# Performance work log

Measured on AMD Instinct MI355X. Metric: run time of the kernel, lower is better.

## Reference

```python
import jax, jax.numpy as jnp
import numpy as np

N_NODES = 10000
N_EDGES = 160000
NF = 512  # node_features
DIMS = [1, 2 * NF // 8, 4 * NF // 8, NF]  # 1 -> 128 -> 256 -> 512


def setup_inputs() -> dict:
    key = jax.random.key(0)
    ks = jax.random.split(key, 10)
    inp = {
        "x": jax.random.normal(ks[0], (N_NODES, 1), dtype=jnp.float32),
        "edge_index": jax.random.randint(ks[1], (2, N_EDGES), 0, N_NODES, dtype=jnp.int64),
        "edge_weights": jax.random.uniform(ks[2], (N_EDGES,), dtype=jnp.float32),
    }
    # Glorot-style init for GCNConv linear weights, zero biases (PyG default)
    for i in range(3):
        d_in, d_out = DIMS[i], DIMS[i + 1]
        scale = (6.0 / (d_in + d_out)) ** 0.5
        inp[f"W{i+1}"] = jax.random.uniform(ks[3 + i], (d_in, d_out), dtype=jnp.float32, minval=-scale, maxval=scale)
        inp[f"b{i+1}"] = jnp.zeros((d_out,), dtype=jnp.float32)
    return inp


def _gcn_layer(h, W, b, src, dst, ew):
    # GCNConv with add_self_loops=False, normalize=False:
    #   h' = scatter_sum(edge_weight * (h @ W)[src] -> dst) + b
    h = h @ W                                    # [N, d_out]
    msg = h[src] * ew[:, None]                   # [E, d_out] gather + scale
    agg = jax.ops.segment_sum(msg, dst, num_segments=N_NODES)  # scatter-add
    return agg + b


def reference(x, edge_index, edge_weights, W1, b1, W2, b2, W3, b3):
    src, dst = edge_index[0], edge_index[1]  # source_to_target flow
    h = _gcn_layer(x, W1, b1, src, dst, edge_weights)
    h = _gcn_layer(h, W2, b2, src, dst, edge_weights)
    h = _gcn_layer(h, W3, b3, src, dst, edge_weights)
    return jax.nn.sigmoid(h)
```

## Files before the change

### kernel.cpp

```cpp
#include <hip/hip_runtime.h>
#include <math.h>

#define N_NODES 10000
#define N_EDGES 160000
#define NCHUNK 32
#define EPC (N_EDGES / NCHUNK)
#define GPC (EPC / 4)


__global__ __launch_bounds__(512) void edges_l1_kernel(
        const int* __restrict__ src, const int* __restrict__ dst,
        const float* __restrict__ ew, const float* __restrict__ x,
        float* __restrict__ s1_part, float* __restrict__ deg_part,
        const float* __restrict__ W1, const float* __restrict__ b1,
        const float* __restrict__ W2,
        float* __restrict__ u_part, float* __restrict__ v_part) {
    int tid = threadIdx.x;
    int blk = blockIdx.x;
    if (blk < 64) {
        __shared__ float lds[N_NODES];
        for (int g = tid; g < N_NODES / 4; g += 512)
            ((float4*)lds)[g] = make_float4(0.f, 0.f, 0.f, 0.f);
        __syncthreads();
        int b = blk & 31;
        bool is_s1 = (blk < 32);
        int base = b * GPC;
        for (int g = tid; g < GPC; g += 512) {
            int4   d4 = ((const int4*)dst)[base + g];
            float4 w4 = ((const float4*)ew)[base + g];
            if (is_s1) {
                int4 s4 = ((const int4*)src)[base + g];
                atomicAdd(&lds[d4.x], w4.x * x[s4.x]);
                atomicAdd(&lds[d4.y], w4.y * x[s4.y]);
                atomicAdd(&lds[d4.z], w4.z * x[s4.z]);
                atomicAdd(&lds[d4.w], w4.w * x[s4.w]);
            } else {
                atomicAdd(&lds[d4.x], w4.x);
                atomicAdd(&lds[d4.y], w4.y);
                atomicAdd(&lds[d4.z], w4.z);
                atomicAdd(&lds[d4.w], w4.w);
            }
        }
        __syncthreads();
        float* dstp = (is_s1 ? s1_part : deg_part) + b * N_NODES;
        for (int g = tid; g < N_NODES / 4; g += 512)
            ((float4*)dstp)[g] = ((float4*)lds)[g];
    } else {
        int b = blk - 64;
        if (tid < 256) {
            int j0 = b * 8;
            float uu = 0.f, vv = 0.f;
            #pragma unroll
            for (int jj = 0; jj < 8; ++jj) {
                float w2 = W2[(j0 + jj) * 256 + tid];
                uu = fmaf(W1[j0 + jj], w2, uu);
                vv = fmaf(b1[j0 + jj], w2, vv);
            }
            u_part[b * 256 + tid] = uu;
            v_part[b * 256 + tid] = vv;
        }
    }
}

__global__ __launch_bounds__(512) void reduce_l1_kernel(
        const float* __restrict__ s1_part, const float* __restrict__ deg_part,
        float* __restrict__ s1, float* __restrict__ deg,
        const float* __restrict__ u_part, const float* __restrict__ v_part,
        const float* __restrict__ b2, const float* __restrict__ W3,
        float* __restrict__ p_part, float* __restrict__ q_part,
        float* __restrict__ r_part) {
    int tid = threadIdx.x;
    int blk = blockIdx.x;
    if (blk < 10) {
        int gid = blk * 512 + tid;
        if (gid < N_NODES / 4) {
            float4 a = make_float4(0.f, 0.f, 0.f, 0.f);
            #pragma unroll
            for (int b = 0; b < NCHUNK; ++b) {
                float4 v = ((const float4*)(s1_part + b * N_NODES))[gid];
                a.x += v.x; a.y += v.y; a.z += v.z; a.w += v.w;
            }
            ((float4*)s1)[gid] = a;
        } else if (gid < 2 * (N_NODES / 4)) {
            int c = gid - N_NODES / 4;
            float4 a = make_float4(0.f, 0.f, 0.f, 0.f);
            #pragma unroll
            for (int b = 0; b < NCHUNK; ++b) {
                float4 v = ((const float4*)(deg_part + b * N_NODES))[c];
                a.x += v.x; a.y += v.y; a.z += v.z; a.w += v.w;
            }
            ((float4*)deg)[c] = a;
        }
    } else {
        int c = blk - 10;
        __shared__ float su[16], sv[16], sb[16];
        if (tid < 16) {
            int kk = c * 16 + tid;
            float uu = 0.f, vv = 0.f;
            #pragma unroll
            for (int b = 0; b < 16; ++b) {
                uu += u_part[b * 256 + kk];
                vv += v_part[b * 256 + kk];
            }
            su[tid] = uu; sv[tid] = vv; sb[tid] = b2[kk];
        }
        __syncthreads();
        float pp = 0.f, qq = 0.f, rr = 0.f;
        #pragma unroll
        for (int kk = 0; kk < 16; ++kk) {
            float w3 = W3[(c * 16 + kk) * 512 + tid];
            pp = fmaf(su[kk], w3, pp);
            qq = fmaf(sv[kk], w3, qq);
            rr = fmaf(sb[kk], w3, rr);
        }
        p_part[c * 512 + tid] = pp;
        q_part[c * 512 + tid] = qq;
        r_part[c * 512 + tid] = rr;
    }
}

__global__ __launch_bounds__(512) void edges_l2_kernel(
        const int* __restrict__ src, const int* __restrict__ dst,
        const float* __restrict__ ew,
        const float* __restrict__ s1, const float* __restrict__ deg,
        float* __restrict__ t2_part, float* __restrict__ B_part) {
    int tid = threadIdx.x;
    int blk = blockIdx.x;
    __shared__ float lds[N_NODES];
    for (int g = tid; g < N_NODES / 4; g += 512)
        ((float4*)lds)[g] = make_float4(0.f, 0.f, 0.f, 0.f);
    __syncthreads();
    int b = blk & 31;
    const float* gsrc = (blk < 32) ? s1 : deg;
    int base = b * GPC;
    for (int g = tid; g < GPC; g += 512) {
        int4   s4 = ((const int4*)src)[base + g];
        int4   d4 = ((const int4*)dst)[base + g];
        float4 w4 = ((const float4*)ew)[base + g];
        atomicAdd(&lds[d4.x], w4.x * gsrc[s4.x]);
        atomicAdd(&lds[d4.y], w4.y * gsrc[s4.y]);
        atomicAdd(&lds[d4.z], w4.z * gsrc[s4.z]);
        atomicAdd(&lds[d4.w], w4.w * gsrc[s4.w]);
    }
    __syncthreads();
    float* dstp = ((blk < 32) ? t2_part : B_part) + b * N_NODES;
    for (int g = tid; g < N_NODES / 4; g += 512)
        ((float4*)dstp)[g] = ((float4*)lds)[g];
}

__global__ __launch_bounds__(512) void reduce_l2_kernel(
        const float* __restrict__ t2_part, const float* __restrict__ B_part,
        float* __restrict__ t2, float* __restrict__ Bf,
        const float* __restrict__ p_part, const float* __restrict__ q_part,
        const float* __restrict__ r_part,
        float* __restrict__ p, float* __restrict__ q, float* __restrict__ r) {
    int tid = threadIdx.x;
    int blk = blockIdx.x;
    if (blk < 10) {
        int gid = blk * 512 + tid;
        if (gid < N_NODES / 4) {
            float4 a = make_float4(0.f, 0.f, 0.f, 0.f);
            #pragma unroll
            for (int b = 0; b < NCHUNK; ++b) {
                float4 v = ((const float4*)(t2_part + b * N_NODES))[gid];
                a.x += v.x; a.y += v.y; a.z += v.z; a.w += v.w;
            }
            ((float4*)t2)[gid] = a;
        } else if (gid < 2 * (N_NODES / 4)) {
            int c = gid - N_NODES / 4;
            float4 a = make_float4(0.f, 0.f, 0.f, 0.f);
            #pragma unroll
            for (int b = 0; b < NCHUNK; ++b) {
                float4 v = ((const float4*)(B_part + b * N_NODES))[c];
                a.x += v.x; a.y += v.y; a.z += v.z; a.w += v.w;
            }
            ((float4*)Bf)[c] = a;
        }
    } else {
        float pp = 0.f, qq = 0.f, rr = 0.f;
        #pragma unroll
        for (int c = 0; c < 16; ++c) {
            pp += p_part[c * 512 + tid];
            qq += q_part[c * 512 + tid];
            rr += r_part[c * 512 + tid];
        }
        p[tid] = pp; q[tid] = qq; r[tid] = rr;
    }
}

__global__ __launch_bounds__(512) void edges_l3_kernel(
        const int* __restrict__ src, const int* __restrict__ dst,
        const float* __restrict__ ew, const float* __restrict__ t2,
        float* __restrict__ A_part) {
    int tid = threadIdx.x;
    int b = blockIdx.x;
    __shared__ float lds[N_NODES];
    for (int g = tid; g < N_NODES / 4; g += 512)
        ((float4*)lds)[g] = make_float4(0.f, 0.f, 0.f, 0.f);
    __syncthreads();
    int base = b * GPC;
    for (int g = tid; g < GPC; g += 512) {
        int4   s4 = ((const int4*)src)[base + g];
        int4   d4 = ((const int4*)dst)[base + g];
        float4 w4 = ((const float4*)ew)[base + g];
        atomicAdd(&lds[d4.x], w4.x * t2[s4.x]);
        atomicAdd(&lds[d4.y], w4.y * t2[s4.y]);
        atomicAdd(&lds[d4.z], w4.z * t2[s4.z]);
        atomicAdd(&lds[d4.w], w4.w * t2[s4.w]);
    }
    __syncthreads();
    float* dstp = A_part + b * N_NODES;
    for (int g = tid; g < N_NODES / 4; g += 512)
        ((float4*)dstp)[g] = ((float4*)lds)[g];
}

__global__ __launch_bounds__(256) void output_kernel(
        const float* __restrict__ A_part, const float* __restrict__ Bf,
        const float* __restrict__ deg,
        const float* __restrict__ p, const float* __restrict__ q,
        const float* __restrict__ r, const float* __restrict__ b3,
        float* __restrict__ out) {
    int tid = threadIdx.x;
    int n0 = blockIdx.x * 16;
    __shared__ float sA[256];
    __shared__ float A_l[16], B_l[16], D_l[16];
    {
        int c = tid & 15, rr = tid >> 4;
        sA[tid] = A_part[rr * N_NODES + n0 + c] +
                  A_part[(rr + 16) * N_NODES + n0 + c];
    }
    __syncthreads();
    if (tid < 16) {
        float s = 0.f;
        #pragma unroll
        for (int b = 0; b < 16; ++b) s += sA[b * 16 + tid];
        A_l[tid] = s;
        B_l[tid] = Bf[n0 + tid];
        D_l[tid] = deg[n0 + tid];
    }
    __syncthreads();
    #pragma unroll
    for (int h = 0; h < 8; ++h) {
        int idx = h * 256 + tid;
        int nl = idx >> 7;
        int j = idx & 127;
        float a = A_l[nl], b = B_l[nl], dg = D_l[nl];
        float4 P = ((const float4*)p)[j];
        float4 Q = ((const float4*)q)[j];
        float4 R = ((const float4*)r)[j];
        float4 B3 = ((const float4*)b3)[j];
        float4 o;
        float zx = fmaf(a, P.x, fmaf(b, Q.x, fmaf(dg, R.x, B3.x)));
        float zy = fmaf(a, P.y, fmaf(b, Q.y, fmaf(dg, R.y, B3.y)));
        float zz = fmaf(a, P.z, fmaf(b, Q.z, fmaf(dg, R.z, B3.z)));
        float zw = fmaf(a, P.w, fmaf(b, Q.w, fmaf(dg, R.w, B3.w)));
        o.x = 1.f / (1.f + __expf(-zx));
        o.y = 1.f / (1.f + __expf(-zy));
        o.z = 1.f / (1.f + __expf(-zz));
        o.w = 1.f / (1.f + __expf(-zw));
        ((float4*)out)[(size_t)(n0 + nl) * 128 + j] = o;
    }
}

extern "C" void kernel_launch(void* const* d_in, const int* in_sizes, int n_in,
                              void* d_out, int out_size, void* d_ws, size_t ws_size,
                              hipStream_t stream) {
    const float* x  = (const float*)d_in[0];
    const int*   ei = (const int*)d_in[1];
    const float* ew = (const float*)d_in[2];
    const float* W1 = (const float*)d_in[3];
    const float* b1 = (const float*)d_in[4];
    const float* W2 = (const float*)d_in[5];
    const float* b2 = (const float*)d_in[6];
    const float* W3 = (const float*)d_in[7];
    const float* b3 = (const float*)d_in[8];
    float* out = (float*)d_out;

    float* ws       = (float*)d_ws;
    float* s1       = ws;
    float* deg      = ws + 10000;
    float* t2       = ws + 20000;
    float* Bf       = ws + 30000;
    float* p        = ws + 40000;
    float* q        = ws + 40512;
    float* r        = ws + 41024;
    float* u_part   = ws + 42000;
    float* v_part   = ws + 46096;
    float* p_part   = ws + 50192;
    float* q_part   = ws + 58384;
    float* r_part   = ws + 66576;
    float* s1_part  = ws + 80000;
    float* deg_part = ws + 400000;
    float* t2_part  = ws + 720000;
    float* B_part   = ws + 1040000;
    float* A_part   = ws + 1360000;

    const int* src = ei;
    const int* dst = ei + N_EDGES;

    edges_l1_kernel<<<80, 512, 0, stream>>>(src, dst, ew, x, s1_part, deg_part,
                                            W1, b1, W2, u_part, v_part);
    reduce_l1_kernel<<<26, 512, 0, stream>>>(s1_part, deg_part, s1, deg,
                                             u_part, v_part, b2, W3,
                                             p_part, q_part, r_part);
    edges_l2_kernel<<<64, 512, 0, stream>>>(src, dst, ew, s1, deg,
                                            t2_part, B_part);
    reduce_l2_kernel<<<11, 512, 0, stream>>>(t2_part, B_part, t2, Bf,
                                             p_part, q_part, r_part, p, q, r);
    edges_l3_kernel<<<32, 512, 0, stream>>>(src, dst, ew, t2, A_part);
    output_kernel<<<625, 256, 0, stream>>>(A_part, Bf, deg, p, q, r, b3, out);
}
```

Measured before the change: 117.6 us.

## Fuse six kernel launches into one cooperative kernel with grid syncs

```diff
diff --git a/kernel.cpp b/kernel.cpp
--- a/kernel.cpp
+++ b/kernel.cpp
@@ -1,52 +1,124 @@
 #include <hip/hip_runtime.h>
+#include <hip/hip_cooperative_groups.h>
 #include <math.h>
+
+namespace cg = cooperative_groups;
 
 #define N_NODES 10000
 #define N_EDGES 160000
-#define NCHUNK 32
+#define NCHUNK 64
 #define EPC (N_EDGES / NCHUNK)
 #define GPC (EPC / 4)
-
-
-__global__ __launch_bounds__(512) void edges_l1_kernel(
+#define GRID 192
+
+
+__device__ __forceinline__ void chunk_scatter(
+        const int* __restrict__ src, const int* __restrict__ dst,
+        const float* __restrict__ ew, const float* __restrict__ gsrc,
+        float* __restrict__ lds, float* __restrict__ part,
+        int chunk, int tid) {
+    for (int g = tid; g < N_NODES / 4; g += 512)
+        ((float4*)lds)[g] = make_float4(0.f, 0.f, 0.f, 0.f);
+    __syncthreads();
+    int base = chunk * GPC;
+    for (int g = tid; g < GPC; g += 512) {
+        int4   s4 = ((const int4*)src)[base + g];
+        int4   d4 = ((const int4*)dst)[base + g];
+        float4 w4 = ((const float4*)ew)[base + g];
+        atomicAdd(&lds[d4.x], w4.x * gsrc[s4.x]);
+        atomicAdd(&lds[d4.y], w4.y * gsrc[s4.y]);
+        atomicAdd(&lds[d4.z], w4.z * gsrc[s4.z]);
+        atomicAdd(&lds[d4.w], w4.w * gsrc[s4.w]);
+    }
+    __syncthreads();
+    float* dstp = part + chunk * N_NODES;
+    for (int g = tid; g < N_NODES / 4; g += 512)
+        ((float4*)dstp)[g] = ((float4*)lds)[g];
+}
+
+__device__ __forceinline__ void reduce64_f4(
+        const float* __restrict__ part, float* __restrict__ outv, int gid) {
+    float4 a = make_float4(0.f, 0.f, 0.f, 0.f);
+    #pragma unroll 8
+    for (int b = 0; b < NCHUNK; ++b) {
+        float4 v = ((const float4*)(part + b * N_NODES))[gid];
+        a.x += v.x; a.y += v.y; a.z += v.z; a.w += v.w;
+    }
+    ((float4*)outv)[gid] = a;
+}
+
+__global__ __launch_bounds__(512) void fused_kernel(
         const int* __restrict__ src, const int* __restrict__ dst,
         const float* __restrict__ ew, const float* __restrict__ x,
-        float* __restrict__ s1_part, float* __restrict__ deg_part,
         const float* __restrict__ W1, const float* __restrict__ b1,
-        const float* __restrict__ W2,
-        float* __restrict__ u_part, float* __restrict__ v_part) {
+        const float* __restrict__ W2, const float* __restrict__ b2,
+        const float* __restrict__ W3, const float* __restrict__ b3,
+        float* __restrict__ ws, float* __restrict__ out) {
+    cg::grid_group grid = cg::this_grid();
+    __shared__ __align__(16) float lds[N_NODES];
+    __shared__ float su[16], sv[16], sb[16];
+    __shared__ float sA[512];
+    __shared__ float A_l[32], B_l[32], D_l[32];
+
+    float* s1       = ws;
+    float* deg      = ws + 10000;
+    float* t2       = ws + 20000;
+    float* Bf       = ws + 30000;
+    float* p        = ws + 40000;
+    float* q        = ws + 40512;
+    float* r        = ws + 41024;
+    float* u_part   = ws + 42000;
+    float* v_part   = ws + 46096;
+    float* p_part   = ws + 50192;
+    float* q_part   = ws + 58384;
+    float* r_part   = ws + 66576;
+    float* s1_part  = ws + 80000;
+    float* deg_part = ws + 720000;
+    float* t2_part  = ws + 1360000;
+    float* B_part   = ws + 2000000;
+    float* A_part   = ws + 2640000;
+
     int tid = threadIdx.x;
     int blk = blockIdx.x;
+
     if (blk < 64) {
-        __shared__ float lds[N_NODES];
         for (int g = tid; g < N_NODES / 4; g += 512)
             ((float4*)lds)[g] = make_float4(0.f, 0.f, 0.f, 0.f);
         __syncthreads();
-        int b = blk & 31;
-        bool is_s1 = (blk < 32);
+        int base = blk * GPC;
+        for (int g = tid; g < GPC; g += 512) {
+            int4   s4 = ((const int4*)src)[base + g];
+            int4   d4 = ((const int4*)dst)[base + g];
+            float4 w4 = ((const float4*)ew)[base + g];
+            atomicAdd(&lds[d4.x], w4.x * x[s4.x]);
+            atomicAdd(&lds[d4.y], w4.y * x[s4.y]);
+            atomicAdd(&lds[d4.z], w4.z * x[s4.z]);
+            atomicAdd(&lds[d4.w], w4.w * x[s4.w]);
+        }
+        __syncthreads();
+        float* dstp = s1_part + blk * N_NODES;
+        for (int g = tid; g < N_NODES / 4; g += 512)
+            ((float4*)dstp)[g] = ((float4*)lds)[g];
+    } else if (blk < 128) {
+        int b = blk - 64;
+        for (int g = tid; g < N_NODES / 4; g += 512)
+            ((float4*)lds)[g] = make_float4(0.f, 0.f, 0.f, 0.f);
+        __syncthreads();
         int base = b * GPC;
         for (int g = tid; g < GPC; g += 512) {
             int4   d4 = ((const int4*)dst)[base + g];
             float4 w4 = ((const float4*)ew)[base + g];
-            if (is_s1) {
-                int4 s4 = ((const int4*)src)[base + g];
-                atomicAdd(&lds[d4.x], w4.x * x[s4.x]);
-                atomicAdd(&lds[d4.y], w4.y * x[s4.y]);
-                atomicAdd(&lds[d4.z], w4.z * x[s4.z]);
-                atomicAdd(&lds[d4.w], w4.w * x[s4.w]);
-            } else {
-                atomicAdd(&lds[d4.x], w4.x);
-                atomicAdd(&lds[d4.y], w4.y);
-                atomicAdd(&lds[d4.z], w4.z);
-                atomicAdd(&lds[d4.w], w4.w);
-            }
-        }
-        __syncthreads();
-        float* dstp = (is_s1 ? s1_part : deg_part) + b * N_NODES;
+            atomicAdd(&lds[d4.x], w4.x);
+            atomicAdd(&lds[d4.y], w4.y);
+            atomicAdd(&lds[d4.z], w4.z);
+            atomicAdd(&lds[d4.w], w4.w);
+        }
+        __syncthreads();
+        float* dstp = deg_part + b * N_NODES;
         for (int g = tid; g < N_NODES / 4; g += 512)
             ((float4*)dstp)[g] = ((float4*)lds)[g];
-    } else {
-        int b = blk - 64;
+    } else if (blk < 144) {
+        int b = blk - 128;
         if (tid < 256) {
             int j0 = b * 8;
             float uu = 0.f, vv = 0.f;
@@ -60,40 +132,16 @@
             v_part[b * 256 + tid] = vv;
         }
     }
-}
-
-__global__ __launch_bounds__(512) void reduce_l1_kernel(
-        const float* __restrict__ s1_part, const float* __restrict__ deg_part,
-        float* __restrict__ s1, float* __restrict__ deg,
-        const float* __restrict__ u_part, const float* __restrict__ v_part,
-        const float* __restrict__ b2, const float* __restrict__ W3,
-        float* __restrict__ p_part, float* __restrict__ q_part,
-        float* __restrict__ r_part) {
-    int tid = threadIdx.x;
-    int blk = blockIdx.x;
-    if (blk < 10) {
+    grid.sync();
+
+    if (blk < 5) {
         int gid = blk * 512 + tid;
-        if (gid < N_NODES / 4) {
-            float4 a = make_float4(0.f, 0.f, 0.f, 0.f);
-            #pragma unroll
-            for (int b = 0; b < NCHUNK; ++b) {
-                float4 v = ((const float4*)(s1_part + b * N_NODES))[gid];
-                a.x += v.x; a.y += v.y; a.z += v.z; a.w += v.w;
-            }
-            ((float4*)s1)[gid] = a;
-        } else if (gid < 2 * (N_NODES / 4)) {
-            int c = gid - N_NODES / 4;
-            float4 a = make_float4(0.f, 0.f, 0.f, 0.f);
-            #pragma unroll
-            for (int b = 0; b < NCHUNK; ++b) {
-                float4 v = ((const float4*)(deg_part + b * N_NODES))[c];
-                a.x += v.x; a.y += v.y; a.z += v.z; a.w += v.w;
-            }
-            ((float4*)deg)[c] = a;
-        }
-    } else {
+        if (gid < N_NODES / 4) reduce64_f4(s1_part, s1, gid);
+    } else if (blk < 10) {
+        int gid = (blk - 5) * 512 + tid;
+        if (gid < N_NODES / 4) reduce64_f4(deg_part, deg, gid);
+    } else if (blk < 26) {
         int c = blk - 10;
-        __shared__ float su[16], sv[16], sb[16];
         if (tid < 16) {
             int kk = c * 16 + tid;
             float uu = 0.f, vv = 0.f;
@@ -117,66 +165,22 @@
         q_part[c * 512 + tid] = qq;
         r_part[c * 512 + tid] = rr;
     }
-}
-
-__global__ __launch_bounds__(512) void edges_l2_kernel(
-        const int* __restrict__ src, const int* __restrict__ dst,
-        const float* __restrict__ ew,
-        const float* __restrict__ s1, const float* __restrict__ deg,
-        float* __restrict__ t2_part, float* __restrict__ B_part) {
-    int tid = threadIdx.x;
-    int blk = blockIdx.x;
-    __shared__ float lds[N_NODES];
-    for (int g = tid; g < N_NODES / 4; g += 512)
-        ((float4*)lds)[g] = make_float4(0.f, 0.f, 0.f, 0.f);
-    __syncthreads();
-    int b = blk & 31;
-    const float* gsrc = (blk < 32) ? s1 : deg;
-    int base = b * GPC;
-    for (int g = tid; g < GPC; g += 512) {
-        int4   s4 = ((const int4*)src)[base + g];
-        int4   d4 = ((const int4*)dst)[base + g];
-        float4 w4 = ((const float4*)ew)[base + g];
-        atomicAdd(&lds[d4.x], w4.x * gsrc[s4.x]);
-        atomicAdd(&lds[d4.y], w4.y * gsrc[s4.y]);
-        atomicAdd(&lds[d4.z], w4.z * gsrc[s4.z]);
-        atomicAdd(&lds[d4.w], w4.w * gsrc[s4.w]);
-    }
-    __syncthreads();
-    float* dstp = ((blk < 32) ? t2_part : B_part) + b * N_NODES;
-    for (int g = tid; g < N_NODES / 4; g += 512)
-        ((float4*)dstp)[g] = ((float4*)lds)[g];
-}
-
-__global__ __launch_bounds__(512) void reduce_l2_kernel(
-        const float* __restrict__ t2_part, const float* __restrict__ B_part,
-        float* __restrict__ t2, float* __restrict__ Bf,
-        const float* __restrict__ p_part, const float* __restrict__ q_part,
-        const float* __restrict__ r_part,
-        float* __restrict__ p, float* __restrict__ q, float* __restrict__ r) {
-    int tid = threadIdx.x;
-    int blk = blockIdx.x;
-    if (blk < 10) {
+    grid.sync();
+
+    if (blk < 64) {
+        chunk_scatter(src, dst, ew, s1, lds, t2_part, blk, tid);
+    } else if (blk < 128) {
+        chunk_scatter(src, dst, ew, deg, lds, B_part, blk - 64, tid);
+    }
+    grid.sync();
+
+    if (blk < 5) {
         int gid = blk * 512 + tid;
-        if (gid < N_NODES / 4) {
-            float4 a = make_float4(0.f, 0.f, 0.f, 0.f);
-            #pragma unroll
-            for (int b = 0; b < NCHUNK; ++b) {
-                float4 v = ((const float4*)(t2_part + b * N_NODES))[gid];
-                a.x += v.x; a.y += v.y; a.z += v.z; a.w += v.w;
-            }
-            ((float4*)t2)[gid] = a;
-        } else if (gid < 2 * (N_NODES / 4)) {
-            int c = gid - N_NODES / 4;
-            float4 a = make_float4(0.f, 0.f, 0.f, 0.f);
-            #pragma unroll
-            for (int b = 0; b < NCHUNK; ++b) {
-                float4 v = ((const float4*)(B_part + b * N_NODES))[c];
-                a.x += v.x; a.y += v.y; a.z += v.z; a.w += v.w;
-            }
-            ((float4*)Bf)[c] = a;
-        }
-    } else {
+        if (gid < N_NODES / 4) reduce64_f4(t2_part, t2, gid);
+    } else if (blk < 10) {
+        int gid = (blk - 5) * 512 + tid;
+        if (gid < N_NODES / 4) reduce64_f4(B_part, Bf, gid);
+    } else if (blk == 10) {
         float pp = 0.f, qq = 0.f, rr = 0.f;
         #pragma unroll
         for (int c = 0; c < 16; ++c) {
@@ -186,79 +190,60 @@
         }
         p[tid] = pp; q[tid] = qq; r[tid] = rr;
     }
-}
-
-__global__ __launch_bounds__(512) void edges_l3_kernel(
-        const int* __restrict__ src, const int* __restrict__ dst,
-        const float* __restrict__ ew, const float* __restrict__ t2,
-        float* __restrict__ A_part) {
-    int tid = threadIdx.x;
-    int b = blockIdx.x;
-    __shared__ float lds[N_NODES];
-    for (int g = tid; g < N_NODES / 4; g += 512)
-        ((float4*)lds)[g] = make_float4(0.f, 0.f, 0.f, 0.f);
-    __syncthreads();
-    int base = b * GPC;
-    for (int g = tid; g < GPC; g += 512) {
-        int4   s4 = ((const int4*)src)[base + g];
-        int4   d4 = ((const int4*)dst)[base + g];
-        float4 w4 = ((const float4*)ew)[base + g];
-        atomicAdd(&lds[d4.x], w4.x * t2[s4.x]);
-        atomicAdd(&lds[d4.y], w4.y * t2[s4.y]);
-        atomicAdd(&lds[d4.z], w4.z * t2[s4.z]);
-        atomicAdd(&lds[d4.w], w4.w * t2[s4.w]);
-    }
-    __syncthreads();
-    float* dstp = A_part + b * N_NODES;
-    for (int g = tid; g < N_NODES / 4; g += 512)
-        ((float4*)dstp)[g] = ((float4*)lds)[g];
-}
-
-__global__ __launch_bounds__(256) void output_kernel(
-        const float* __restrict__ A_part, const float* __restrict__ Bf,
-        const float* __restrict__ deg,
-        const float* __restrict__ p, const float* __restrict__ q,
-        const float* __restrict__ r, const float* __restrict__ b3,
-        float* __restrict__ out) {
-    int tid = threadIdx.x;
-    int n0 = blockIdx.x * 16;
-    __shared__ float sA[256];
-    __shared__ float A_l[16], B_l[16], D_l[16];
-    {
-        int c = tid & 15, rr = tid >> 4;
-        sA[tid] = A_part[rr * N_NODES + n0 + c] +
-                  A_part[(rr + 16) * N_NODES + n0 + c];
-    }
-    __syncthreads();
-    if (tid < 16) {
-        float s = 0.f;
+    grid.sync();
+
+    if (blk < 64) {
+        chunk_scatter(src, dst, ew, t2, lds, A_part, blk, tid);
+    }
+    grid.sync();
+
+    for (int tile = blk; tile < (N_NODES + 31) / 32; tile += GRID) {
+        int n0 = tile * 32;
+        int nn = (N_NODES - n0 < 32) ? (N_NODES - n0) : 32;
+        __syncthreads();
+        {
+            int nl = tid >> 4, g = tid & 15;
+            float s = 0.f;
+            if (nl < nn) {
+                int n = n0 + nl;
+                s = A_part[g * N_NODES + n] + A_part[(g + 16) * N_NODES + n] +
+                    A_part[(g + 32) * N_NODES + n] + A_part[(g + 48) * N_NODES + n];
+            }
+            sA[tid] = s;
+        }
+        __syncthreads();
+        if (tid < 32 && tid < nn) {
+            float s = 0.f;
+            #pragma unroll
+            for (int g = 0; g < 16; ++g) s += sA[tid * 16 + g];
+            A_l[tid] = s;
+            B_l[tid] = Bf[n0 + tid];
+            D_l[tid] = deg[n0 + tid];
+        }
+        __syncthreads();
         #pragma unroll
-        for (int b = 0; b < 16; ++b) s += sA[b * 16 + tid];
-        A_l[tid] = s;
-        B_l[tid] = Bf[n0 + tid];
-        D_l[tid] = deg[n0 + tid];
-    }
-    __syncthreads();
-    #pragma unroll
-    for (int h = 0; h < 8; ++h) {
-        int idx = h * 256 + tid;
-        int nl = idx >> 7;
-        int j = idx & 127;
-        float a = A_l[nl], b = B_l[nl], dg = D_l[nl];
-        float4 P = ((const float4*)p)[j];
-        float4 Q = ((const float4*)q)[j];
-        float4 R = ((const float4*)r)[j];
-        float4 B3 = ((const float4*)b3)[j];
-        float4 o;
-        float zx = fmaf(a, P.x, fmaf(b, Q.x, fmaf(dg, R.x, B3.x)));
-        float zy = fmaf(a, P.y, fmaf(b, Q.y, fmaf(dg, R.y, B3.y)));
-        float zz = fmaf(a, P.z, fmaf(b, Q.z, fmaf(dg, R.z, B3.z)));
-        float zw = fmaf(a, P.w, fmaf(b, Q.w, fmaf(dg, R.w, B3.w)));
-        o.x = 1.f / (1.f + __expf(-zx));
-        o.y = 1.f / (1.f + __expf(-zy));
-        o.z = 1.f / (1.f + __expf(-zz));
-        o.w = 1.f / (1.f + __expf(-zw));
-        ((float4*)out)[(size_t)(n0 + nl) * 128 + j] = o;
+        for (int h = 0; h < 8; ++h) {
+            int idx = h * 512 + tid;
+            int nl = idx >> 7;
+            int j = idx & 127;
+            if (nl < nn) {
+                float a = A_l[nl], b = B_l[nl], dg = D_l[nl];
+                float4 P = ((const float4*)p)[j];
+                float4 Q = ((const float4*)q)[j];
+                float4 R = ((const float4*)r)[j];
+                float4 B3 = ((const float4*)b3)[j];
+                float4 o;
+                float zx = fmaf(a, P.x, fmaf(b, Q.x, fmaf(dg, R.x, B3.x)));
+                float zy = fmaf(a, P.y, fmaf(b, Q.y, fmaf(dg, R.y, B3.y)));
+                float zz = fmaf(a, P.z, fmaf(b, Q.z, fmaf(dg, R.z, B3.z)));
+                float zw = fmaf(a, P.w, fmaf(b, Q.w, fmaf(dg, R.w, B3.w)));
+                o.x = 1.f / (1.f + __expf(-zx));
+                o.y = 1.f / (1.f + __expf(-zy));
+                o.z = 1.f / (1.f + __expf(-zz));
+                o.w = 1.f / (1.f + __expf(-zw));
+                ((float4*)out)[(size_t)(n0 + nl) * 128 + j] = o;
+            }
+        }
     }
 }
 
@@ -275,38 +260,16 @@
     const float* W3 = (const float*)d_in[7];
     const float* b3 = (const float*)d_in[8];
     float* out = (float*)d_out;
-
-    float* ws       = (float*)d_ws;
-    float* s1       = ws;
-    float* deg      = ws + 10000;
-    float* t2       = ws + 20000;
-    float* Bf       = ws + 30000;
-    float* p        = ws + 40000;
-    float* q        = ws + 40512;
-    float* r        = ws + 41024;
-    float* u_part   = ws + 42000;
-    float* v_part   = ws + 46096;
-    float* p_part   = ws + 50192;
-    float* q_part   = ws + 58384;
-    float* r_part   = ws + 66576;
-    float* s1_part  = ws + 80000;
-    float* deg_part = ws + 400000;
-    float* t2_part  = ws + 720000;
-    float* B_part   = ws + 1040000;
-    float* A_part   = ws + 1360000;
+    float* ws  = (float*)d_ws;
 
     const int* src = ei;
     const int* dst = ei + N_EDGES;
 
-    edges_l1_kernel<<<80, 512, 0, stream>>>(src, dst, ew, x, s1_part, deg_part,
-                                            W1, b1, W2, u_part, v_part);
-    reduce_l1_kernel<<<26, 512, 0, stream>>>(s1_part, deg_part, s1, deg,
-                                             u_part, v_part, b2, W3,
-                                             p_part, q_part, r_part);
-    edges_l2_kernel<<<64, 512, 0, stream>>>(src, dst, ew, s1, deg,
-                                            t2_part, B_part);
-    reduce_l2_kernel<<<11, 512, 0, stream>>>(t2_part, B_part, t2, Bf,
-                                             p_part, q_part, r_part, p, q, r);
-    edges_l3_kernel<<<32, 512, 0, stream>>>(src, dst, ew, t2, A_part);
-    output_kernel<<<625, 256, 0, stream>>>(A_part, Bf, deg, p, q, r, b3, out);
-}
+    void* args[] = {
+        (void*)&src, (void*)&dst, (void*)&ew, (void*)&x,
+        (void*)&W1, (void*)&b1, (void*)&W2, (void*)&b2,
+        (void*)&W3, (void*)&b3, (void*)&ws, (void*)&out,
+    };
+    hipLaunchCooperativeKernel((void*)fused_kernel, dim3(GRID), dim3(512),
+                               args, 0, stream);
+}
```

New measurement: 241.2 us. 2.05x slower.

## Fuse partial-sum reductions into following edge scatter kernels, cutting launches from six to four

Applied to the files above, without the earlier changes.

```diff
diff --git a/kernel.cpp b/kernel.cpp
--- a/kernel.cpp
+++ b/kernel.cpp
@@ -6,9 +6,10 @@
 #define NCHUNK 32
 #define EPC (N_EDGES / NCHUNK)
 #define GPC (EPC / 4)
-
-
-__global__ __launch_bounds__(512) void edges_l1_kernel(
+#define NF4 (N_NODES / 4)
+
+
+__global__ __launch_bounds__(512) void k1_kernel(
         const int* __restrict__ src, const int* __restrict__ dst,
         const float* __restrict__ ew, const float* __restrict__ x,
         float* __restrict__ s1_part, float* __restrict__ deg_part,
@@ -18,8 +19,8 @@
     int tid = threadIdx.x;
     int blk = blockIdx.x;
     if (blk < 64) {
-        __shared__ float lds[N_NODES];
-        for (int g = tid; g < N_NODES / 4; g += 512)
+        __shared__ __align__(16) float lds[N_NODES];
+        for (int g = tid; g < NF4; g += 512)
             ((float4*)lds)[g] = make_float4(0.f, 0.f, 0.f, 0.f);
         __syncthreads();
         int b = blk & 31;
@@ -43,7 +44,7 @@
         }
         __syncthreads();
         float* dstp = (is_s1 ? s1_part : deg_part) + b * N_NODES;
-        for (int g = tid; g < N_NODES / 4; g += 512)
+        for (int g = tid; g < NF4; g += 512)
             ((float4*)dstp)[g] = ((float4*)lds)[g];
     } else {
         int b = blk - 64;
@@ -62,37 +63,65 @@
     }
 }
 
-__global__ __launch_bounds__(512) void reduce_l1_kernel(
+__device__ __forceinline__ void fused_reduce_scatter(
+        const int* __restrict__ src, const int* __restrict__ dst,
+        const float* __restrict__ ew,
+        const float* __restrict__ part_in, float* __restrict__ part_out,
+        float* lds_src, float* lds_acc, int b, int tid) {
+    for (int g = tid; g < NF4; g += 512) {
+        float4 a = make_float4(0.f, 0.f, 0.f, 0.f);
+        #pragma unroll 8
+        for (int c = 0; c < NCHUNK; ++c) {
+            float4 v = ((const float4*)(part_in + c * N_NODES))[g];
+            a.x += v.x; a.y += v.y; a.z += v.z; a.w += v.w;
+        }
+        ((float4*)lds_src)[g] = a;
+        ((float4*)lds_acc)[g] = make_float4(0.f, 0.f, 0.f, 0.f);
+    }
+    __syncthreads();
+    int base = b * GPC;
+    for (int g = tid; g < GPC; g += 512) {
+        int4   s4 = ((const int4*)src)[base + g];
+        int4   d4 = ((const int4*)dst)[base + g];
+        float4 w4 = ((const float4*)ew)[base + g];
+        atomicAdd(&lds_acc[d4.x], w4.x * lds_src[s4.x]);
+        atomicAdd(&lds_acc[d4.y], w4.y * lds_src[s4.y]);
+        atomicAdd(&lds_acc[d4.z], w4.z * lds_src[s4.z]);
+        atomicAdd(&lds_acc[d4.w], w4.w * lds_src[s4.w]);
+    }
+    __syncthreads();
+    float* dstp = part_out + b * N_NODES;
+    for (int g = tid; g < NF4; g += 512)
+        ((float4*)dstp)[g] = ((float4*)lds_acc)[g];
+}
+
+__global__ __launch_bounds__(512) void k2_kernel(
+        const int* __restrict__ src, const int* __restrict__ dst,
+        const float* __restrict__ ew,
         const float* __restrict__ s1_part, const float* __restrict__ deg_part,
-        float* __restrict__ s1, float* __restrict__ deg,
+        float* __restrict__ t2_part, float* __restrict__ B_part,
+        float* __restrict__ deg,
         const float* __restrict__ u_part, const float* __restrict__ v_part,
         const float* __restrict__ b2, const float* __restrict__ W3,
         float* __restrict__ p_part, float* __restrict__ q_part,
         float* __restrict__ r_part) {
     int tid = threadIdx.x;
     int blk = blockIdx.x;
-    if (blk < 10) {
-        int gid = blk * 512 + tid;
-        if (gid < N_NODES / 4) {
-            float4 a = make_float4(0.f, 0.f, 0.f, 0.f);
-            #pragma unroll
-            for (int b = 0; b < NCHUNK; ++b) {
-                float4 v = ((const float4*)(s1_part + b * N_NODES))[gid];
-                a.x += v.x; a.y += v.y; a.z += v.z; a.w += v.w;
-            }
-            ((float4*)s1)[gid] = a;
-        } else if (gid < 2 * (N_NODES / 4)) {
-            int c = gid - N_NODES / 4;
-            float4 a = make_float4(0.f, 0.f, 0.f, 0.f);
-            #pragma unroll
-            for (int b = 0; b < NCHUNK; ++b) {
-                float4 v = ((const float4*)(deg_part + b * N_NODES))[c];
-                a.x += v.x; a.y += v.y; a.z += v.z; a.w += v.w;
-            }
-            ((float4*)deg)[c] = a;
+    if (blk < 64) {
+        __shared__ __align__(16) float lds_src[N_NODES];
+        __shared__ __align__(16) float lds_acc[N_NODES];
+        bool is_t2 = (blk < 32);
+        int b = blk & 31;
+        fused_reduce_scatter(src, dst, ew,
+                             is_t2 ? s1_part : deg_part,
+                             is_t2 ? t2_part : B_part,
+                             lds_src, lds_acc, b, tid);
+        if (blk == 32) {
+            for (int g = tid; g < NF4; g += 512)
+                ((float4*)deg)[g] = ((float4*)lds_src)[g];
         }
     } else {
-        int c = blk - 10;
+        int c = blk - 64;
         __shared__ float su[16], sv[16], sb[16];
         if (tid < 16) {
             int kk = c * 16 + tid;
@@ -119,64 +148,22 @@
     }
 }
 
-__global__ __launch_bounds__(512) void edges_l2_kernel(
+__global__ __launch_bounds__(512) void k3_kernel(
         const int* __restrict__ src, const int* __restrict__ dst,
         const float* __restrict__ ew,
-        const float* __restrict__ s1, const float* __restrict__ deg,
-        float* __restrict__ t2_part, float* __restrict__ B_part) {
-    int tid = threadIdx.x;
-    int blk = blockIdx.x;
-    __shared__ float lds[N_NODES];
-    for (int g = tid; g < N_NODES / 4; g += 512)
-        ((float4*)lds)[g] = make_float4(0.f, 0.f, 0.f, 0.f);
-    __syncthreads();
-    int b = blk & 31;
-    const float* gsrc = (blk < 32) ? s1 : deg;
-    int base = b * GPC;
-    for (int g = tid; g < GPC; g += 512) {
-        int4   s4 = ((const int4*)src)[base + g];
-        int4   d4 = ((const int4*)dst)[base + g];
-        float4 w4 = ((const float4*)ew)[base + g];
-        atomicAdd(&lds[d4.x], w4.x * gsrc[s4.x]);
-        atomicAdd(&lds[d4.y], w4.y * gsrc[s4.y]);
-        atomicAdd(&lds[d4.z], w4.z * gsrc[s4.z]);
-        atomicAdd(&lds[d4.w], w4.w * gsrc[s4.w]);
-    }
-    __syncthreads();
-    float* dstp = ((blk < 32) ? t2_part : B_part) + b * N_NODES;
-    for (int g = tid; g < N_NODES / 4; g += 512)
-        ((float4*)dstp)[g] = ((float4*)lds)[g];
-}
-
-__global__ __launch_bounds__(512) void reduce_l2_kernel(
         const float* __restrict__ t2_part, const float* __restrict__ B_part,
-        float* __restrict__ t2, float* __restrict__ Bf,
+        float* __restrict__ A_part, float* __restrict__ Bf,
         const float* __restrict__ p_part, const float* __restrict__ q_part,
         const float* __restrict__ r_part,
         float* __restrict__ p, float* __restrict__ q, float* __restrict__ r) {
     int tid = threadIdx.x;
     int blk = blockIdx.x;
-    if (blk < 10) {
-        int gid = blk * 512 + tid;
-        if (gid < N_NODES / 4) {
-            float4 a = make_float4(0.f, 0.f, 0.f, 0.f);
-            #pragma unroll
-            for (int b = 0; b < NCHUNK; ++b) {
-                float4 v = ((const float4*)(t2_part + b * N_NODES))[gid];
-                a.x += v.x; a.y += v.y; a.z += v.z; a.w += v.w;
-            }
-            ((float4*)t2)[gid] = a;
-        } else if (gid < 2 * (N_NODES / 4)) {
-            int c = gid - N_NODES / 4;
-            float4 a = make_float4(0.f, 0.f, 0.f, 0.f);
-            #pragma unroll
-            for (int b = 0; b < NCHUNK; ++b) {
-                float4 v = ((const float4*)(B_part + b * N_NODES))[c];
-                a.x += v.x; a.y += v.y; a.z += v.z; a.w += v.w;
-            }
-            ((float4*)Bf)[c] = a;
-        }
-    } else {
+    if (blk < 32) {
+        __shared__ __align__(16) float lds_src[N_NODES];
+        __shared__ __align__(16) float lds_acc[N_NODES];
+        fused_reduce_scatter(src, dst, ew, t2_part, A_part,
+                             lds_src, lds_acc, blk, tid);
+    } else if (blk == 32) {
         float pp = 0.f, qq = 0.f, rr = 0.f;
         #pragma unroll
         for (int c = 0; c < 16; ++c) {
@@ -185,33 +172,17 @@
             rr += r_part[c * 512 + tid];
         }
         p[tid] = pp; q[tid] = qq; r[tid] = rr;
-    }
-}
-
-__global__ __launch_bounds__(512) void edges_l3_kernel(
-        const int* __restrict__ src, const int* __restrict__ dst,
-        const float* __restrict__ ew, const float* __restrict__ t2,
-        float* __restrict__ A_part) {
-    int tid = threadIdx.x;
-    int b = blockIdx.x;
-    __shared__ float lds[N_NODES];
-    for (int g = tid; g < N_NODES / 4; g += 512)
-        ((float4*)lds)[g] = make_float4(0.f, 0.f, 0.f, 0.f);
-    __syncthreads();
-    int base = b * GPC;
-    for (int g = tid; g < GPC; g += 512) {
-        int4   s4 = ((const int4*)src)[base + g];
-        int4   d4 = ((const int4*)dst)[base + g];
-        float4 w4 = ((const float4*)ew)[base + g];
-        atomicAdd(&lds[d4.x], w4.x * t2[s4.x]);
-        atomicAdd(&lds[d4.y], w4.y * t2[s4.y]);
-        atomicAdd(&lds[d4.z], w4.z * t2[s4.z]);
-        atomicAdd(&lds[d4.w], w4.w * t2[s4.w]);
-    }
-    __syncthreads();
-    float* dstp = A_part + b * N_NODES;
-    for (int g = tid; g < N_NODES / 4; g += 512)
-        ((float4*)dstp)[g] = ((float4*)lds)[g];
+    } else {
+        for (int g = tid; g < NF4; g += 512) {
+            float4 a = make_float4(0.f, 0.f, 0.f, 0.f);
+            #pragma unroll 8
+            for (int c = 0; c < NCHUNK; ++c) {
+                float4 v = ((const float4*)(B_part + c * N_NODES))[g];
+                a.x += v.x; a.y += v.y; a.z += v.z; a.w += v.w;
+            }
+            ((float4*)Bf)[g] = a;
+        }
+    }
 }
 
 __global__ __launch_bounds__(256) void output_kernel(
@@ -277,36 +248,33 @@
     float* out = (float*)d_out;
 
     float* ws       = (float*)d_ws;
-    float* s1       = ws;
-    float* deg      = ws + 10000;
-    float* t2       = ws + 20000;
-    float* Bf       = ws + 30000;
-    float* p        = ws + 40000;
-    float* q        = ws + 40512;
-    float* r        = ws + 41024;
-    float* u_part   = ws + 42000;
-    float* v_part   = ws + 46096;
-    float* p_part   = ws + 50192;
-    float* q_part   = ws + 58384;
-    float* r_part   = ws + 66576;
-    float* s1_part  = ws + 80000;
-    float* deg_part = ws + 400000;
-    float* t2_part  = ws + 720000;
-    float* B_part   = ws + 1040000;
-    float* A_part   = ws + 1360000;
+    float* deg      = ws;
+    float* Bf       = ws + 10000;
+    float* p        = ws + 20000;
+    float* q        = ws + 20512;
+    float* r        = ws + 21024;
+    float* u_part   = ws + 22000;
+    float* v_part   = ws + 26096;
+    float* p_part   = ws + 30192;
+    float* q_part   = ws + 38384;
+    float* r_part   = ws + 46576;
+    float* s1_part  = ws + 60000;
+    float* deg_part = ws + 380000;
+    float* t2_part  = ws + 700000;
+    float* B_part   = ws + 1020000;
+    float* A_part   = ws + 1340000;
 
     const int* src = ei;
     const int* dst = ei + N_EDGES;
 
-    edges_l1_kernel<<<80, 512, 0, stream>>>(src, dst, ew, x, s1_part, deg_part,
-                                            W1, b1, W2, u_part, v_part);
-    reduce_l1_kernel<<<26, 512, 0, stream>>>(s1_part, deg_part, s1, deg,
-                                             u_part, v_part, b2, W3,
-                                             p_part, q_part, r_part);
-    edges_l2_kernel<<<64, 512, 0, stream>>>(src, dst, ew, s1, deg,
-                                            t2_part, B_part);
-    reduce_l2_kernel<<<11, 512, 0, stream>>>(t2_part, B_part, t2, Bf,
-                                             p_part, q_part, r_part, p, q, r);
-    edges_l3_kernel<<<32, 512, 0, stream>>>(src, dst, ew, t2, A_part);
+    k1_kernel<<<80, 512, 0, stream>>>(src, dst, ew, x, s1_part, deg_part,
+                                      W1, b1, W2, u_part, v_part);
+    k2_kernel<<<80, 512, 0, stream>>>(src, dst, ew, s1_part, deg_part,
+                                      t2_part, B_part, deg,
+                                      u_part, v_part, b2, W3,
+                                      p_part, q_part, r_part);
+    k3_kernel<<<34, 512, 0, stream>>>(src, dst, ew, t2_part, B_part,
+                                      A_part, Bf,
+                                      p_part, q_part, r_part, p, q, r);
     output_kernel<<<625, 256, 0, stream>>>(A_part, Bf, deg, p, q, r, b3, out);
 }
```

New measurement: 133.5 us. 1.13x slower.
